# Optimization experiments

Hardware: AMD Instinct MI355X
Metric: run time of the kernel (lower is better)

The kernel has to match this reference:

```python
import jax, jax.numpy as jnp
import numpy as np

B, N, M = 64, 4096, 128


def setup_inputs() -> dict:
    key = jax.random.key(0)
    x = jax.random.normal(key, (B, N, M), dtype=jnp.float32)
    return {"x": x}


def reference(x):
    # Original loops over channels M, applying a 1D FFT along the N axis to
    # each (batch, N) slice. Equivalent batched form: FFT along axis=1.
    f = jnp.fft.fft(x.astype(jnp.complex64), axis=1)  # (B, N, M) complex64
    return (jnp.real(f), jnp.imag(f))
```

## Files before the change

kernel.cpp:

```cpp
#include <hip/hip_runtime.h>
#include <hip/hip_fp16.h>

#define B 64
#define N 4096
#define M 128

constexpr int T    = 1024;
constexpr int CPB  = 16;
constexpr int NF   = 8;
constexpr int NWG  = B * (M / CPB);

__device__ __forceinline__ int fold5(int p) {
    return (p & ~31) | ((p ^ (p >> 5) ^ (p >> 9)) & 31);
}
__device__ __forceinline__ int rev12(int k) {
    return ((k & 7) << 9) | (((k >> 3) & 7) << 6) | (((k >> 6) & 7) << 3) | ((k >> 9) & 7);
}

__device__ __forceinline__ float2 cadd(float2 a, float2 b){ return make_float2(a.x+b.x, a.y+b.y); }
__device__ __forceinline__ float2 csub(float2 a, float2 b){ return make_float2(a.x-b.x, a.y-b.y); }
__device__ __forceinline__ float2 cmul(float2 a, float2 b){ return make_float2(a.x*b.x - a.y*b.y, a.x*b.y + a.y*b.x); }
__device__ __forceinline__ float2 mulnegi(float2 a){ return make_float2(a.y, -a.x); }
__device__ __forceinline__ float2 muli(float2 a)  { return make_float2(-a.y, a.x); }
__device__ __forceinline__ float2 cis(float ang){ float s, c; __sincosf(ang, &s, &c); return make_float2(c, s); }
__device__ __forceinline__ float2 h2f(__half2 h){ return __half22float2(h); }
__device__ __forceinline__ __half2 f2h(float2 v){ return __floats2half2_rn(v.x, v.y); }

__device__ __forceinline__ void dft8(float2 t[8]) {
    float2 e0=cadd(t[0],t[4]), e1=csub(t[0],t[4]);
    float2 e2=cadd(t[2],t[6]), e3=csub(t[2],t[6]);
    float2 E0=cadd(e0,e2), E2=csub(e0,e2);
    float2 E1=cadd(e1,mulnegi(e3)), E3=cadd(e1,muli(e3));
    float2 o0=cadd(t[1],t[5]), o1=csub(t[1],t[5]);
    float2 o2=cadd(t[3],t[7]), o3=csub(t[3],t[7]);
    float2 O0=cadd(o0,o2), O2=csub(o0,o2);
    float2 O1=cadd(o1,mulnegi(o3)), O3=cadd(o1,muli(o3));
    const float C = 0.70710678118654752f;
    float2 w1O1 = make_float2(C*(O1.x+O1.y), C*(O1.y-O1.x));
    float2 w2O2 = mulnegi(O2);
    float2 w3O3 = make_float2(C*(O3.y-O3.x), -C*(O3.x+O3.y));
    t[0]=cadd(E0,O0);   t[4]=csub(E0,O0);
    t[1]=cadd(E1,w1O1); t[5]=csub(E1,w1O1);
    t[2]=cadd(E2,w2O2); t[6]=csub(E2,w2O2);
    t[3]=cadd(E3,w3O3); t[7]=csub(E3,w3O3);
}

template<int S>
__device__ __forceinline__ void stage(__half2* z, int tid) {
    #pragma unroll
    for (int it = 0; it < 4; ++it) {
        const int q  = tid + (it << 10);
        const int f  = q >> 9;
        const int qq = q & 511;
        int G, j;
        if      (S == 512) { G = 0;                j = qq;      }
        else if (S == 64)  { G = (qq >> 6) << 9;   j = qq & 63; }
        else if (S == 8)   { G = (qq >> 3) << 6;   j = qq & 7;  }
        else               { G = qq << 3;          j = 0;       }
        const int nbase = G + j;
        const int fb = f << 12;
        int idx[8];
        #pragma unroll
        for (int c = 0; c < 8; ++c) idx[c] = fb + fold5(nbase + c * S);
        float2 r[8];
        #pragma unroll
        for (int c = 0; c < 8; ++c) r[c] = h2f(z[idx[c]]);
        dft8(r);
        if (S > 1) {
            float2 w1 = cis(-6.2831853071795864f * (float)j / (float)(8 * S));
            float2 w = w1;
            #pragma unroll
            for (int k = 1; k < 8; ++k) { r[k] = cmul(r[k], w); w = cmul(w, w1); }
        }
        #pragma unroll
        for (int c = 0; c < 8; ++c) z[idx[c]] = f2h(r[c]);
    }
}

__global__ __launch_bounds__(T, 4)
void fft_one(const float* __restrict__ x, float* __restrict__ out) {
    extern __shared__ __half2 z[];
    const int bid = blockIdx.x;
    const int b = bid >> 3, mg = bid & 7;
    const int m0 = mg * CPB;
    const float* xb = x + (size_t)b * N * M + m0;
    const int tid = threadIdx.x;

    #pragma unroll
    for (int it = 0; it < 16; ++it) {
        int i = tid + (it << 10);
        int n = i >> 2, c = i & 3;
        float4 v = *(const float4*)(xb + (size_t)n * M + (c << 2));
        int fn = fold5(n);
        z[((2 * c)     << 12) + fn] = f2h(make_float2(v.x, v.y));
        z[((2 * c + 1) << 12) + fn] = f2h(make_float2(v.z, v.w));
    }
    __syncthreads();

    stage<512>(z, tid); __syncthreads();
    stage<64 >(z, tid); __syncthreads();
    stage<8  >(z, tid); __syncthreads();
    stage<1  >(z, tid); __syncthreads();

    float* outRe = out;
    float* outIm = out + (size_t)B * N * M;
    const size_t rbase = (size_t)b * N * M + m0;
    #pragma unroll
    for (int it = 0; it < 16; ++it) {
        int u = tid + (it << 10);
        int k = u >> 2, c = u & 3;
        int kk = (N - k) & (N - 1);
        int sk = fold5(rev12(k)), smk = fold5(rev12(kk));
        int f0 = (2 * c) << 12, f1 = (2 * c + 1) << 12;
        float2 Zk0 = h2f(z[f0 + sk]),  Zm0 = h2f(z[f0 + smk]);
        float2 Zk1 = h2f(z[f1 + sk]),  Zm1 = h2f(z[f1 + smk]);
        float4 re, im;
        re.x = 0.5f * (Zk0.x + Zm0.x); im.x = 0.5f * (Zk0.y - Zm0.y);
        re.y = 0.5f * (Zk0.y + Zm0.y); im.y = 0.5f * (Zm0.x - Zk0.x);
        re.z = 0.5f * (Zk1.x + Zm1.x); im.z = 0.5f * (Zk1.y - Zm1.y);
        re.w = 0.5f * (Zk1.y + Zm1.y); im.w = 0.5f * (Zm1.x - Zk1.x);
        *(float4*)(outRe + rbase + (size_t)k * M + (c << 2)) = re;
        *(float4*)(outIm + rbase + (size_t)k * M + (c << 2)) = im;
    }
}

extern "C" void kernel_launch(void* const* d_in, const int* in_sizes, int n_in,
                              void* d_out, int out_size, void* d_ws, size_t ws_size,
                              hipStream_t stream) {
    const float* x = (const float*)d_in[0];
    float* out = (float*)d_out;
    const int lds_bytes = NF * N * (int)sizeof(__half2);
    hipFuncSetAttribute((const void*)fft_one,
                        hipFuncAttributeMaxDynamicSharedMemorySize, lds_bytes);
    fft_one<<<NWG, T, lds_bytes, stream>>>(x, out);
}
```

Before: 146.1 us.

## Halve workgroup size and channel tile, remap block order, skew LDS banks per FFT

Each workgroup now handles 8 channels (4 packed complex FFTs) with 512 threads and 64 KB of LDS instead of 16 channels, 1024 threads and 128 KB. This should let more workgroups be resident per CU. The block index is remapped so consecutive blocks cover 8 batches of the same channel group, which changes the DRAM access order. The LDS swizzle also XORs the FFT index into the bank bits, which should cut bank conflicts when threads touch different packed FFTs. Each 32-byte global row segment is now narrower, which may lower coalescing efficiency.

```diff
diff --git a/kernel.cpp b/kernel.cpp
--- a/kernel.cpp
+++ b/kernel.cpp
@@ -5,13 +5,15 @@
 #define N 4096
 #define M 128
 
-constexpr int T    = 1024;
-constexpr int CPB  = 16;
-constexpr int NF   = 8;
-constexpr int NWG  = B * (M / CPB);
+constexpr int T    = 512;
+constexpr int CPB  = 8;
+constexpr int NF   = 4;
+constexpr int NGB  = M / CPB;
+constexpr int NWG  = B * NGB;
 
-__device__ __forceinline__ int fold5(int p) {
-    return (p & ~31) | ((p ^ (p >> 5) ^ (p >> 9)) & 31);
+__device__ __forceinline__ int slot(int f, int p) {
+    int low = (p ^ (p >> 5) ^ (p >> 9) ^ (f << 3)) & 31;
+    return (f << 12) + (p & ~31) + low;
 }
 __device__ __forceinline__ int rev12(int k) {
     return ((k & 7) << 9) | (((k >> 3) & 7) << 6) | (((k >> 6) & 7) << 3) | ((k >> 9) & 7);
@@ -49,7 +51,7 @@
 __device__ __forceinline__ void stage(__half2* z, int tid) {
     #pragma unroll
     for (int it = 0; it < 4; ++it) {
-        const int q  = tid + (it << 10);
+        const int q  = tid + (it << 9);
         const int f  = q >> 9;
         const int qq = q & 511;
         int G, j;
@@ -58,10 +60,9 @@
         else if (S == 8)   { G = (qq >> 3) << 6;   j = qq & 7;  }
         else               { G = qq << 3;          j = 0;       }
         const int nbase = G + j;
-        const int fb = f << 12;
         int idx[8];
         #pragma unroll
-        for (int c = 0; c < 8; ++c) idx[c] = fb + fold5(nbase + c * S);
+        for (int c = 0; c < 8; ++c) idx[c] = slot(f, nbase + c * S);
         float2 r[8];
         #pragma unroll
         for (int c = 0; c < 8; ++c) r[c] = h2f(z[idx[c]]);
@@ -80,20 +81,21 @@
 __global__ __launch_bounds__(T, 4)
 void fft_one(const float* __restrict__ x, float* __restrict__ out) {
     extern __shared__ __half2 z[];
+
     const int bid = blockIdx.x;
-    const int b = bid >> 3, mg = bid & 7;
-    const int m0 = mg * CPB;
+    const int b  = ((bid >> 7) << 3) | (bid & 7);
+    const int g  = (bid >> 3) & 15;
+    const int m0 = g * CPB;
     const float* xb = x + (size_t)b * N * M + m0;
     const int tid = threadIdx.x;
 
     #pragma unroll
     for (int it = 0; it < 16; ++it) {
-        int i = tid + (it << 10);
-        int n = i >> 2, c = i & 3;
+        int i = tid + (it << 9);
+        int n = i >> 1, c = i & 1;
         float4 v = *(const float4*)(xb + (size_t)n * M + (c << 2));
-        int fn = fold5(n);
-        z[((2 * c)     << 12) + fn] = f2h(make_float2(v.x, v.y));
-        z[((2 * c + 1) << 12) + fn] = f2h(make_float2(v.z, v.w));
+        z[slot(2 * c,     n)] = f2h(make_float2(v.x, v.y));
+        z[slot(2 * c + 1, n)] = f2h(make_float2(v.z, v.w));
     }
     __syncthreads();
 
@@ -107,13 +109,14 @@
     const size_t rbase = (size_t)b * N * M + m0;
     #pragma unroll
     for (int it = 0; it < 16; ++it) {
-        int u = tid + (it << 10);
-        int k = u >> 2, c = u & 3;
+        int u = tid + (it << 9);
+        int k = u >> 1, c = u & 1;
         int kk = (N - k) & (N - 1);
-        int sk = fold5(rev12(k)), smk = fold5(rev12(kk));
-        int f0 = (2 * c) << 12, f1 = (2 * c + 1) << 12;
-        float2 Zk0 = h2f(z[f0 + sk]),  Zm0 = h2f(z[f0 + smk]);
-        float2 Zk1 = h2f(z[f1 + sk]),  Zm1 = h2f(z[f1 + smk]);
+        int sk = rev12(k), smk = rev12(kk);
+        float2 Zk0 = h2f(z[slot(2 * c,     sk )]);
+        float2 Zm0 = h2f(z[slot(2 * c,     smk)]);
+        float2 Zk1 = h2f(z[slot(2 * c + 1, sk )]);
+        float2 Zm1 = h2f(z[slot(2 * c + 1, smk)]);
         float4 re, im;
         re.x = 0.5f * (Zk0.x + Zm0.x); im.x = 0.5f * (Zk0.y - Zm0.y);
         re.y = 0.5f * (Zk0.y + Zm0.y); im.y = 0.5f * (Zm0.x - Zk0.x);
```

Result: slower. 158.6 us (+8.6%).

## Interleave four FFT columns per LDS element for 128-bit accesses and shared twiddles

Applied to the files above, without the earlier changes.

The shared-memory layout now packs four complex half2 columns into each 16-byte element, so every FFT stage thread does eight uint4 LDS loads and stores and runs four radix-8 butterflies that reuse one set of twiddles. This cuts the count of LDS instructions and twiddle sincos/cmul work per butterfly. The bank swizzle is reworked for the wider elements, and the block-to-(batch, channel-group) mapping is permuted, which may change L2/DRAM locality. Register pressure rises because each thread holds 32 complex values at once, which could hurt occupancy.

```diff
diff --git a/kernel.cpp b/kernel.cpp
--- a/kernel.cpp
+++ b/kernel.cpp
@@ -5,13 +5,12 @@
 #define N 4096
 #define M 128
 
-constexpr int T    = 1024;
-constexpr int CPB  = 16;
-constexpr int NF   = 8;
-constexpr int NWG  = B * (M / CPB);
+constexpr int T   = 1024;
+constexpr int CPB = 16;
+constexpr int NWG = B * (M / CPB);
 
-__device__ __forceinline__ int fold5(int p) {
-    return (p & ~31) | ((p ^ (p >> 5) ^ (p >> 9)) & 31);
+__device__ __forceinline__ int sidx(int p) {
+    return (p & ~7) | ((p ^ (p >> 3) ^ (p >> 6) ^ (p >> 9)) & 7);
 }
 __device__ __forceinline__ int rev12(int k) {
     return ((k & 7) << 9) | (((k >> 3) & 7) << 6) | (((k >> 6) & 7) << 3) | ((k >> 9) & 7);
@@ -25,6 +24,8 @@
 __device__ __forceinline__ float2 cis(float ang){ float s, c; __sincosf(ang, &s, &c); return make_float2(c, s); }
 __device__ __forceinline__ float2 h2f(__half2 h){ return __half22float2(h); }
 __device__ __forceinline__ __half2 f2h(float2 v){ return __floats2half2_rn(v.x, v.y); }
+__device__ __forceinline__ unsigned h2u(__half2 h){ return *(unsigned*)&h; }
+__device__ __forceinline__ __half2 u2h(unsigned u){ return *(__half2*)&u; }
 
 __device__ __forceinline__ void dft8(float2 t[8]) {
     float2 e0=cadd(t[0],t[4]), e1=csub(t[0],t[4]);
@@ -46,43 +47,55 @@
 }
 
 template<int S>
-__device__ __forceinline__ void stage(__half2* z, int tid) {
+__device__ __forceinline__ void stage(uint4* zp, int tid) {
+    const int g  = tid >> 9;
+    const int qq = tid & 511;
+    int G, j;
+    if      (S == 512) { G = 0;               j = qq;      }
+    else if (S == 64)  { G = (qq >> 6) << 9;  j = qq & 63; }
+    else if (S == 8)   { G = (qq >> 3) << 6;  j = qq & 7;  }
+    else               { G = qq << 3;         j = 0;       }
+    const int base = g << 12;
+    int idx[8];
+    uint4 leg[8];
     #pragma unroll
-    for (int it = 0; it < 4; ++it) {
-        const int q  = tid + (it << 10);
-        const int f  = q >> 9;
-        const int qq = q & 511;
-        int G, j;
-        if      (S == 512) { G = 0;                j = qq;      }
-        else if (S == 64)  { G = (qq >> 6) << 9;   j = qq & 63; }
-        else if (S == 8)   { G = (qq >> 3) << 6;   j = qq & 7;  }
-        else               { G = qq << 3;          j = 0;       }
-        const int nbase = G + j;
-        const int fb = f << 12;
-        int idx[8];
+    for (int c = 0; c < 8; ++c) {
+        idx[c] = base + sidx(G + j + c * S);
+        leg[c] = zp[idx[c]];
+    }
+    float2 w[8];
+    if (S > 1) {
+        float2 w1 = cis(-6.2831853071795864f * (float)j / (float)(8 * S));
+        w[1] = w1;
         #pragma unroll
-        for (int c = 0; c < 8; ++c) idx[c] = fb + fold5(nbase + c * S);
-        float2 r[8];
+        for (int k = 2; k < 8; ++k) w[k] = cmul(w[k-1], w1);
+    }
+    #pragma unroll
+    for (int pl = 0; pl < 4; ++pl) {
+        float2 t[8];
         #pragma unroll
-        for (int c = 0; c < 8; ++c) r[c] = h2f(z[idx[c]]);
-        dft8(r);
+        for (int c = 0; c < 8; ++c) t[c] = h2f(u2h(((unsigned*)&leg[c])[pl]));
+        dft8(t);
         if (S > 1) {
-            float2 w1 = cis(-6.2831853071795864f * (float)j / (float)(8 * S));
-            float2 w = w1;
             #pragma unroll
-            for (int k = 1; k < 8; ++k) { r[k] = cmul(r[k], w); w = cmul(w, w1); }
+            for (int k = 1; k < 8; ++k) t[k] = cmul(t[k], w[k]);
         }
         #pragma unroll
-        for (int c = 0; c < 8; ++c) z[idx[c]] = f2h(r[c]);
+        for (int c = 0; c < 8; ++c) ((unsigned*)&leg[c])[pl] = h2u(f2h(t[c]));
     }
+    #pragma unroll
+    for (int c = 0; c < 8; ++c) zp[idx[c]] = leg[c];
 }
 
 __global__ __launch_bounds__(T, 4)
 void fft_one(const float* __restrict__ x, float* __restrict__ out) {
-    extern __shared__ __half2 z[];
+    extern __shared__ __align__(16) unsigned char lds_raw[];
+    uint4* zp = (uint4*)lds_raw;
+    uint2* z2 = (uint2*)lds_raw;
+
     const int bid = blockIdx.x;
-    const int b = bid >> 3, mg = bid & 7;
-    const int m0 = mg * CPB;
+    const int b  = ((bid >> 6) << 3) | (bid & 7);
+    const int m0 = ((bid >> 3) & 7) * CPB;
     const float* xb = x + (size_t)b * N * M + m0;
     const int tid = threadIdx.x;
 
@@ -91,16 +104,18 @@
         int i = tid + (it << 10);
         int n = i >> 2, c = i & 3;
         float4 v = *(const float4*)(xb + (size_t)n * M + (c << 2));
-        int fn = fold5(n);
-        z[((2 * c)     << 12) + fn] = f2h(make_float2(v.x, v.y));
-        z[((2 * c + 1) << 12) + fn] = f2h(make_float2(v.z, v.w));
+        int g = c >> 1, h = c & 1;
+        uint2 wv;
+        wv.x = h2u(f2h(make_float2(v.x, v.y)));
+        wv.y = h2u(f2h(make_float2(v.z, v.w)));
+        z2[(g << 13) + sidx(n) * 2 + h] = wv;
     }
     __syncthreads();
 
-    stage<512>(z, tid); __syncthreads();
-    stage<64 >(z, tid); __syncthreads();
-    stage<8  >(z, tid); __syncthreads();
-    stage<1  >(z, tid); __syncthreads();
+    stage<512>(zp, tid); __syncthreads();
+    stage<64 >(zp, tid); __syncthreads();
+    stage<8  >(zp, tid); __syncthreads();
+    stage<1  >(zp, tid); __syncthreads();
 
     float* outRe = out;
     float* outIm = out + (size_t)B * N * M;
@@ -110,10 +125,13 @@
         int u = tid + (it << 10);
         int k = u >> 2, c = u & 3;
         int kk = (N - k) & (N - 1);
-        int sk = fold5(rev12(k)), smk = fold5(rev12(kk));
-        int f0 = (2 * c) << 12, f1 = (2 * c + 1) << 12;
-        float2 Zk0 = h2f(z[f0 + sk]),  Zm0 = h2f(z[f0 + smk]);
-        float2 Zk1 = h2f(z[f1 + sk]),  Zm1 = h2f(z[f1 + smk]);
+        int g = c >> 1, h = c & 1;
+        int sk  = sidx(rev12(k));
+        int smk = sidx(rev12(kk));
+        uint2 a  = z2[(g << 13) + sk  * 2 + h];
+        uint2 bq = z2[(g << 13) + smk * 2 + h];
+        float2 Zk0 = h2f(u2h(a.x)),  Zk1 = h2f(u2h(a.y));
+        float2 Zm0 = h2f(u2h(bq.x)), Zm1 = h2f(u2h(bq.y));
         float4 re, im;
         re.x = 0.5f * (Zk0.x + Zm0.x); im.x = 0.5f * (Zk0.y - Zm0.y);
         re.y = 0.5f * (Zk0.y + Zm0.y); im.y = 0.5f * (Zm0.x - Zk0.x);
@@ -129,7 +147,7 @@
                               hipStream_t stream) {
     const float* x = (const float*)d_in[0];
     float* out = (float*)d_out;
-    const int lds_bytes = NF * N * (int)sizeof(__half2);
+    const int lds_bytes = 2 * N * 16;
     hipFuncSetAttribute((const void*)fft_one,
                         hipFuncAttributeMaxDynamicSharedMemorySize, lds_bytes);
     fft_one<<<NWG, T, lds_bytes, stream>>>(x, out);
```

Result: slower. 168.0 us (+15.0%).

## Process two channel groups per workgroup with register prefetch of the second group

Applied to the files above, without the earlier changes.

Halves the grid to 256 workgroups, each handling two 16-channel groups of the same batch one after the other. The second group's input is prefetched into registers while the first is computed, so load latency overlaps with compute. The LDS swizzle now also XORs in the frame index to spread bank conflicts across frames. The 64 extra VGPRs of prefetch may hurt occupancy under the 1024-thread launch bound, and 256 workgroups exactly fill the 256 CUs, giving less latency hiding than eight workgroups per CU.

```diff
diff --git a/kernel.cpp b/kernel.cpp
--- a/kernel.cpp
+++ b/kernel.cpp
@@ -5,13 +5,12 @@
 #define N 4096
 #define M 128
 
-constexpr int T    = 1024;
-constexpr int CPB  = 16;
-constexpr int NF   = 8;
-constexpr int NWG  = B * (M / CPB);
+constexpr int T   = 1024;
+constexpr int CPB = 16;
+constexpr int NWG = 256;
 
-__device__ __forceinline__ int fold5(int p) {
-    return (p & ~31) | ((p ^ (p >> 5) ^ (p >> 9)) & 31);
+__device__ __forceinline__ int slot(int f, int p) {
+    return (f << 12) + (p & ~31) + ((p ^ (p >> 5) ^ (p >> 9) ^ (f << 2)) & 31);
 }
 __device__ __forceinline__ int rev12(int k) {
     return ((k & 7) << 9) | (((k >> 3) & 7) << 6) | (((k >> 6) & 7) << 3) | ((k >> 9) & 7);
@@ -49,19 +48,18 @@
 __device__ __forceinline__ void stage(__half2* z, int tid) {
     #pragma unroll
     for (int it = 0; it < 4; ++it) {
-        const int q  = tid + (it << 10);
-        const int f  = q >> 9;
-        const int qq = q & 511;
+        const int qv = tid + (it << 10);
+        const int f  = qv >> 9;
+        const int qq = qv & 511;
         int G, j;
-        if      (S == 512) { G = 0;                j = qq;      }
-        else if (S == 64)  { G = (qq >> 6) << 9;   j = qq & 63; }
-        else if (S == 8)   { G = (qq >> 3) << 6;   j = qq & 7;  }
-        else               { G = qq << 3;          j = 0;       }
+        if      (S == 512) { G = 0;               j = qq;      }
+        else if (S == 64)  { G = (qq >> 6) << 9;  j = qq & 63; }
+        else if (S == 8)   { G = (qq >> 3) << 6;  j = qq & 7;  }
+        else               { G = qq << 3;         j = 0;       }
         const int nbase = G + j;
-        const int fb = f << 12;
         int idx[8];
         #pragma unroll
-        for (int c = 0; c < 8; ++c) idx[c] = fb + fold5(nbase + c * S);
+        for (int c = 0; c < 8; ++c) idx[c] = slot(f, nbase + c * S);
         float2 r[8];
         #pragma unroll
         for (int c = 0; c < 8; ++c) r[c] = h2f(z[idx[c]]);
@@ -77,43 +75,26 @@
     }
 }
 
-__global__ __launch_bounds__(T, 4)
-void fft_one(const float* __restrict__ x, float* __restrict__ out) {
-    extern __shared__ __half2 z[];
-    const int bid = blockIdx.x;
-    const int b = bid >> 3, mg = bid & 7;
-    const int m0 = mg * CPB;
-    const float* xb = x + (size_t)b * N * M + m0;
-    const int tid = threadIdx.x;
-
-    #pragma unroll
-    for (int it = 0; it < 16; ++it) {
-        int i = tid + (it << 10);
-        int n = i >> 2, c = i & 3;
-        float4 v = *(const float4*)(xb + (size_t)n * M + (c << 2));
-        int fn = fold5(n);
-        z[((2 * c)     << 12) + fn] = f2h(make_float2(v.x, v.y));
-        z[((2 * c + 1) << 12) + fn] = f2h(make_float2(v.z, v.w));
-    }
-    __syncthreads();
-
+__device__ __forceinline__ void run_stages(__half2* z, int tid) {
     stage<512>(z, tid); __syncthreads();
     stage<64 >(z, tid); __syncthreads();
     stage<8  >(z, tid); __syncthreads();
     stage<1  >(z, tid); __syncthreads();
+}
 
-    float* outRe = out;
-    float* outIm = out + (size_t)B * N * M;
-    const size_t rbase = (size_t)b * N * M + m0;
+__device__ __forceinline__ void unpack_store(const __half2* z, int tid,
+                                             float* outRe, float* outIm,
+                                             size_t rbase) {
     #pragma unroll
     for (int it = 0; it < 16; ++it) {
         int u = tid + (it << 10);
         int k = u >> 2, c = u & 3;
         int kk = (N - k) & (N - 1);
-        int sk = fold5(rev12(k)), smk = fold5(rev12(kk));
-        int f0 = (2 * c) << 12, f1 = (2 * c + 1) << 12;
-        float2 Zk0 = h2f(z[f0 + sk]),  Zm0 = h2f(z[f0 + smk]);
-        float2 Zk1 = h2f(z[f1 + sk]),  Zm1 = h2f(z[f1 + smk]);
+        int rk = rev12(k), rm = rev12(kk);
+        float2 Zk0 = h2f(z[slot(2*c,   rk)]);
+        float2 Zm0 = h2f(z[slot(2*c,   rm)]);
+        float2 Zk1 = h2f(z[slot(2*c+1, rk)]);
+        float2 Zm1 = h2f(z[slot(2*c+1, rm)]);
         float4 re, im;
         re.x = 0.5f * (Zk0.x + Zm0.x); im.x = 0.5f * (Zk0.y - Zm0.y);
         re.y = 0.5f * (Zk0.y + Zm0.y); im.y = 0.5f * (Zm0.x - Zk0.x);
@@ -124,12 +105,63 @@
     }
 }
 
+__global__ __launch_bounds__(T, 4)
+void fft_one(const float* __restrict__ x, float* __restrict__ out) {
+    extern __shared__ __half2 z[];
+
+    const int bid = blockIdx.x;
+    const int b   = ((bid >> 5) << 3) | (bid & 7);
+    const int qb  = (bid >> 3) & 3;
+    const int tid = threadIdx.x;
+
+    const int m0_0 = qb * CPB;
+    const int m0_1 = (qb + 4) * CPB;
+    const float* xb0 = x + (size_t)b * N * M + m0_0;
+    const float* xb1 = x + (size_t)b * N * M + m0_1;
+    float* outRe = out;
+    float* outIm = out + (size_t)B * N * M;
+
+    #pragma unroll
+    for (int it = 0; it < 16; ++it) {
+        int i = tid + (it << 10);
+        int n = i >> 2, c = i & 3;
+        float4 v = *(const float4*)(xb0 + (size_t)n * M + (c << 2));
+        z[slot(2*c,   n)] = f2h(make_float2(v.x, v.y));
+        z[slot(2*c+1, n)] = f2h(make_float2(v.z, v.w));
+    }
+    float4 pf[16];
+    #pragma unroll
+    for (int it = 0; it < 16; ++it) {
+        int i = tid + (it << 10);
+        int n = i >> 2, c = i & 3;
+        pf[it] = *(const float4*)(xb1 + (size_t)n * M + (c << 2));
+    }
+    __syncthreads();
+
+    run_stages(z, tid);
+    unpack_store(z, tid, outRe, outIm, (size_t)b * N * M + m0_0);
+    __syncthreads();
+
+    #pragma unroll
+    for (int it = 0; it < 16; ++it) {
+        int i = tid + (it << 10);
+        int n = i >> 2, c = i & 3;
+        float4 v = pf[it];
+        z[slot(2*c,   n)] = f2h(make_float2(v.x, v.y));
+        z[slot(2*c+1, n)] = f2h(make_float2(v.z, v.w));
+    }
+    __syncthreads();
+
+    run_stages(z, tid);
+    unpack_store(z, tid, outRe, outIm, (size_t)b * N * M + m0_1);
+}
+
 extern "C" void kernel_launch(void* const* d_in, const int* in_sizes, int n_in,
                               void* d_out, int out_size, void* d_ws, size_t ws_size,
                               hipStream_t stream) {
     const float* x = (const float*)d_in[0];
     float* out = (float*)d_out;
-    const int lds_bytes = NF * N * (int)sizeof(__half2);
+    const int lds_bytes = 8 * N * (int)sizeof(__half2);
     hipFuncSetAttribute((const void*)fft_one,
                         hipFuncAttributeMaxDynamicSharedMemorySize, lds_bytes);
     fft_one<<<NWG, T, lds_bytes, stream>>>(x, out);
```

After: 330.3 us. 126% more time.
